# Kernel tuning notes

Measured on AMD Instinct MI355X. Metric: run time of the kernel, lower is better.

The kernel has to match this reference:

```python
import jax, jax.numpy as jnp
import numpy as np

REL_DIM = 1024
NUM_HEADS = 16
HEAD_DIM = REL_DIM // NUM_HEADS
REL_EMB_DIM = 256
B, K = 32, 512
SCALE = 1.0 / float(np.sqrt(HEAD_DIM))


def setup_inputs() -> dict:
    key = jax.random.key(0)
    ks = jax.random.split(key, 7)
    s = 1.0 / float(np.sqrt(REL_DIM))
    return {
        "h_R": jax.random.normal(ks[0], (B, K, REL_DIM), dtype=jnp.float32),
        "R": jax.random.normal(ks[1], (K, REL_EMB_DIM), dtype=jnp.float32),
        "W_q": jax.random.normal(ks[2], (REL_DIM, REL_DIM), dtype=jnp.float32) * s,
        "W_k": jax.random.normal(ks[3], (REL_DIM, REL_DIM), dtype=jnp.float32) * s,
        "W_v": jax.random.normal(ks[4], (REL_DIM, REL_DIM), dtype=jnp.float32) * s,
        "W_o": jax.random.normal(ks[5], (REL_DIM, REL_DIM), dtype=jnp.float32) * s,
        "w_sim": jax.random.normal(ks[6], (NUM_HEADS,), dtype=jnp.float32) * 0.1,
    }


def reference(h_R, R, W_q, W_k, W_v, W_o, w_sim):
    Bb, Kk, _ = h_R.shape
    H, D = NUM_HEADS, HEAD_DIM
    # torch Linear: x @ W.T ; then split heads -> (B, H, K, D)
    def proj(x, W):
        return jnp.einsum('bkd,ed->bke', x, W).reshape(Bb, Kk, H, D).transpose(0, 2, 1, 3)
    q = proj(h_R, W_q)
    k = proj(h_R, W_k)
    v = proj(h_R, W_v)
    attn = jnp.einsum('bhqd,bhkd->bhqk', q, k) * SCALE
    # cosine-similarity bias (batch-independent): (H, K, K)
    R_norm = R / jnp.maximum(jnp.linalg.norm(R, axis=-1, keepdims=True), 1e-12)
    sim = R_norm @ R_norm.T  # (K, K)
    bias = w_sim[:, None, None] * sim[None]  # (H, K, K)
    attn = attn + bias[None]
    alpha = jax.nn.softmax(attn, axis=-1)
    out = jnp.einsum('bhqk,bhkd->bhqd', alpha, v)
    out = out.transpose(0, 2, 1, 3).reshape(Bb, Kk, H * D)
    return jnp.einsum('bkd,ed->bke', out, W_o)
```

## Files before the change

### kernel.cpp

```cpp
#include <hip/hip_runtime.h>

#define SEQK 512
#define NH 16
#define HD 64
#define RD 1024
#define BBATCH 32
#define QK_SCALE 0.125f
#define LOG2E 1.4426950408889634f

typedef unsigned short u16;
using bf16x8 = __attribute__((ext_vector_type(8))) short;
using f32x4  = __attribute__((ext_vector_type(4))) float;

__device__ __forceinline__ u16 f2bf(float f) {
  unsigned u = __float_as_uint(f);
  u += 0x7FFFu + ((u >> 16) & 1u);
  return (u16)(u >> 16);
}
__device__ __forceinline__ float bf2f(u16 v) {
  return __uint_as_float(((unsigned)v) << 16);
}
__device__ __forceinline__ float fexp2(float x) {
  float r;
  asm("v_exp_f32 %0, %1" : "=v"(r) : "v"(x));
  return r;
}

__device__ __forceinline__ void async_cp16(const void* g, void* l) {
  __builtin_amdgcn_global_load_lds(
      (__attribute__((address_space(1))) void*)(void*)g,
      (__attribute__((address_space(3))) void*)l,
      16, 0, 0);
}

__global__ void convert_kernel(const float* __restrict__ hR,
                               const float* __restrict__ Wq, const float* __restrict__ Wk,
                               const float* __restrict__ Wv, const float* __restrict__ Wo,
                               u16* __restrict__ hR16,
                               u16* __restrict__ Wq16, u16* __restrict__ Wk16,
                               u16* __restrict__ Wv16, u16* __restrict__ Wo16) {
  size_t i4 = (size_t)blockIdx.x * blockDim.x + threadIdx.x;
  size_t e = i4 * 4;
  const float* src; u16* dst; size_t off;
  if (e < 16777216u) { src = hR; dst = hR16; off = e; }
  else {
    size_t r = e - 16777216u;
    int w = (int)(r >> 20);
    off = r & 1048575u;
    src = (w == 0 ? Wq : w == 1 ? Wk : w == 2 ? Wv : Wo);
    dst = (w == 0 ? Wq16 : w == 1 ? Wk16 : w == 2 ? Wv16 : Wo16);
  }
  float4 v = *(const float4*)(src + off);
  ushort4 o;
  o.x = f2bf(v.x); o.y = f2bf(v.y); o.z = f2bf(v.z); o.w = f2bf(v.w);
  *(ushort4*)(dst + off) = o;
}

__global__ void rnorm_kernel(const float* __restrict__ R, float* __restrict__ Rn) {
  int row = blockIdx.x;
  int lane = threadIdx.x;
  float4 v = *(const float4*)(R + (size_t)row * 256 + lane * 4);
  float ss = v.x * v.x + v.y * v.y + v.z * v.z + v.w * v.w;
  for (int off = 32; off; off >>= 1) ss += __shfl_xor(ss, off);
  float s = 1.0f / fmaxf(sqrtf(ss), 1e-12f);
  float4 o = {v.x * s, v.y * s, v.z * s, v.w * s};
  *(float4*)(Rn + (size_t)row * 256 + lane * 4) = o;
}

__global__ void sim_kernel(const float* __restrict__ Rn, u16* __restrict__ sim16) {
  __shared__ float Rl[16 * 256];
  int i0 = blockIdx.x * 16;
  int t = threadIdx.x;
  #pragma unroll
  for (int i = 0; i < 4; i++) {
    int f = t + i * 256;
    *(float4*)&Rl[f * 4] = *(const float4*)(Rn + (size_t)i0 * 256 + f * 4);
  }
  __syncthreads();
  for (int jj = 0; jj < 2; jj++) {
    int j = jj * 256 + t;
    float acc[16];
    #pragma unroll
    for (int i = 0; i < 16; i++) acc[i] = 0.f;
    for (int c = 0; c < 64; c++) {
      float4 rv = *(const float4*)(Rn + (size_t)j * 256 + c * 4);
      #pragma unroll
      for (int i = 0; i < 16; i++) {
        float4 a = *(const float4*)&Rl[i * 256 + c * 4];
        acc[i] += a.x * rv.x + a.y * rv.y + a.z * rv.z + a.w * rv.w;
      }
    }
    #pragma unroll
    for (int i = 0; i < 16; i++) sim16[(size_t)(i0 + i) * 512 + j] = f2bf(acc[i]);
  }
}

template <int MODE>
__global__ __launch_bounds__(256)
void gemm_kernel(const u16* __restrict__ A,
                 const u16* __restrict__ B0, const u16* __restrict__ B1,
                 const u16* __restrict__ B2,
                 u16* __restrict__ q16, u16* __restrict__ k16, u16* __restrict__ v16,
                 float* __restrict__ outF) {
  __shared__ u16 Alds[128 * 32];
  __shared__ u16 Blds[128 * 32];
  int tid = threadIdx.x;
  int wave = tid >> 6, lane = tid & 63;
  int wm = wave & 1, wn = wave >> 1;
  int lr = lane & 15, qd = lane >> 4;
  int mb = blockIdx.x * 128;
  int ny = blockIdx.y;

  const u16* Bmat;
  int nbmat;
  if (MODE == 0) {
    int wsel = ny >> 3;
    Bmat = (wsel == 0 ? B0 : wsel == 1 ? B1 : B2);
    nbmat = (ny & 7) * 128;
  } else {
    Bmat = B0;
    nbmat = ny * 128;
  }

  f32x4 zero = {0.f, 0.f, 0.f, 0.f};
  f32x4 acc[4][4];
  #pragma unroll
  for (int i = 0; i < 4; i++)
    #pragma unroll
    for (int j = 0; j < 4; j++) acc[i][j] = zero;

  for (int kb = 0; kb < 1024; kb += 32) {
    #pragma unroll
    for (int j = 0; j < 2; j++) {
      int r = (wave * 2 + j) * 16 + (lane >> 2);
      int c = (lane & 3) ^ ((r >> 1) & 3);
      async_cp16(A + (size_t)(mb + r) * 1024 + kb + c * 8,
                 &Alds[(wave * 2 + j) * 512]);
      async_cp16(Bmat + (size_t)(nbmat + r) * 1024 + kb + c * 8,
                 &Blds[(wave * 2 + j) * 512]);
    }
    __syncthreads();

    bf16x8 af[4], bf[4];
    #pragma unroll
    for (int mi = 0; mi < 4; mi++) {
      int ra = wm * 64 + mi * 16 + lr;
      af[mi] = *(const bf16x8*)&Alds[ra * 32 + ((qd ^ ((ra >> 1) & 3)) << 3)];
      int rb = wn * 64 + mi * 16 + lr;
      bf[mi] = *(const bf16x8*)&Blds[rb * 32 + ((qd ^ ((rb >> 1) & 3)) << 3)];
    }
    #pragma unroll
    for (int mi = 0; mi < 4; mi++)
      #pragma unroll
      for (int ni = 0; ni < 4; ni++)
        acc[mi][ni] = __builtin_amdgcn_mfma_f32_16x16x32_bf16(af[mi], bf[ni],
                                                              acc[mi][ni], 0, 0, 0);
    __syncthreads();
  }

  if (MODE == 0) {
    int wsel = ny >> 3;
    u16* dst = (wsel == 0 ? q16 : wsel == 1 ? k16 : v16);
    float scl = (wsel == 0) ? QK_SCALE * LOG2E : 1.0f;
    #pragma unroll
    for (int mi = 0; mi < 4; mi++) {
      int m = mb + wm * 64 + mi * 16 + qd * 4;
      int b = m >> 9, kk = m & 511;
      #pragma unroll
      for (int ni = 0; ni < 4; ni++) {
        int n = nbmat + wn * 64 + ni * 16 + lr;
        int h = n >> 6, d = n & 63;
        u16* p = dst + ((size_t)(b * 16 + h) * 512 + kk) * 64 + d;
        #pragma unroll
        for (int r = 0; r < 4; r++) p[(size_t)r * 64] = f2bf(acc[mi][ni][r] * scl);
      }
    }
  } else {
    #pragma unroll
    for (int mi = 0; mi < 4; mi++) {
      int m = mb + wm * 64 + mi * 16 + qd * 4;
      #pragma unroll
      for (int ni = 0; ni < 4; ni++) {
        int n = ny * 128 + wn * 64 + ni * 16 + lr;
        #pragma unroll
        for (int r = 0; r < 4; r++) outF[(size_t)(m + r) * 1024 + n] = acc[mi][ni][r];
      }
    }
  }
}

__global__ void vtrans_kernel(const u16* __restrict__ v16, u16* __restrict__ vt16) {
  __shared__ u16 tile[64 * 72];
  int kt = blockIdx.x;
  int bh = blockIdx.y;
  int t = threadIdx.x;
  const u16* src = v16 + ((size_t)bh * 512 + kt * 64) * 64;
  #pragma unroll
  for (int j = 0; j < 2; j++) {
    int linear = j * 2048 + t * 8;
    int kr = linear >> 6, d0 = linear & 63;
    bf16x8 vv = *(const bf16x8*)(src + (size_t)kr * 64 + d0);
    #pragma unroll
    for (int e = 0; e < 8; e++) tile[kr * 72 + d0 + e] = (u16)vv[e];
  }
  __syncthreads();
  #pragma unroll
  for (int j = 0; j < 2; j++) {
    int linear = j * 2048 + t * 8;
    int dr = linear >> 6, k0 = linear & 63;
    bf16x8 ov;
    #pragma unroll
    for (int e = 0; e < 8; e++) ov[e] = (short)tile[(k0 + e) * 72 + dr];
    *(bf16x8*)(vt16 + ((size_t)bh * 64 + dr) * 512 + kt * 64 + k0) = ov;
  }
}

__global__ __launch_bounds__(256, 2)
void attn_kernel(const u16* __restrict__ q16, const u16* __restrict__ k16,
                 const u16* __restrict__ vt16, const u16* __restrict__ sim16,
                 const float* __restrict__ wsim, u16* __restrict__ attn16) {
  __shared__ u16 Kbuf[2][128 * 64];
  __shared__ u16 Vbuf[2][64 * 128];
  __shared__ u16 Plds[4 * 16 * 128];

  int id = blockIdx.x;
  int xcd = id & 7;
  int j = id >> 3;
  int qt = j & 7;
  int bh = xcd * 64 + (j >> 3);
  int b = bh >> 4, h = bh & 15;

  int tid = threadIdx.x;
  int wave = tid >> 6, lane = tid & 63;
  int lr = lane & 15, qd = lane >> 4;
  int qrb = qt * 64 + wave * 16;
  u16* Pw = &Plds[wave * 2048];

  const u16* qp = q16 + ((size_t)bh * 512 + qrb + lr) * 64 + qd * 8;
  bf16x8 aq0 = *(const bf16x8*)qp;
  bf16x8 aq1 = *(const bf16x8*)(qp + 32);

  float ws = wsim[h] * LOG2E;
  int row0 = qrb + qd * 4;

  f32x4 zero = {0.f, 0.f, 0.f, 0.f};
  f32x4 o[4];
  #pragma unroll
  for (int nt = 0; nt < 4; nt++) o[nt] = zero;
  float m_run[4] = {-1e30f, -1e30f, -1e30f, -1e30f};
  float l_run[4] = {0.f, 0.f, 0.f, 0.f};

  const u16* kbase = k16 + (size_t)bh * 512 * 64;
  const u16* vbase = vt16 + (size_t)bh * 64 * 512;

  auto stage = [&](int nb, int ck) {
    int k0 = ck * 128;
    #pragma unroll
    for (int jj = 0; jj < 4; jj++) {
      int rbase = wave * 32 + jj * 8;
      int r = rbase + (lane >> 3);
      int c = (lane & 7) ^ (r & 7);
      async_cp16(kbase + (size_t)(k0 + r) * 64 + c * 8, &Kbuf[nb][rbase * 64]);
    }
    #pragma unroll
    for (int jj = 0; jj < 4; jj++) {
      int dbase = wave * 16 + jj * 4;
      int d = dbase + (lane >> 4);
      int c = (lane & 15) ^ (d & 15);
      async_cp16(vbase + (size_t)d * 512 + k0 + c * 8, &Vbuf[nb][dbase * 128]);
    }
  };

  stage(0, 0);
  __syncthreads();

  int cb = 0;
  for (int ck = 0; ck < 4; ck++) {
    int k0 = ck * 128;

    ushort4 braw[8];
    #pragma unroll
    for (int jt = 0; jt < 8; jt++) {
      int kl = jt * 16 + lr;
      braw[jt] = *(const ushort4*)(sim16 + (size_t)(k0 + kl) * 512 + row0);
    }
    __builtin_amdgcn_sched_barrier(0);
    if (ck < 3) stage(cb ^ 1, ck + 1);

    const u16* Kc = &Kbuf[cb][0];
    const u16* Vc = &Vbuf[cb][0];

    __builtin_amdgcn_s_setprio(1);
    f32x4 s[8];
    #pragma unroll
    for (int jt = 0; jt < 8; jt++) {
      int kl = jt * 16 + lr;
      ushort4 b4 = braw[jt];
      f32x4 t = {ws * bf2f(b4.x), ws * bf2f(b4.y), ws * bf2f(b4.z), ws * bf2f(b4.w)};
      const u16* krow = Kc + kl * 64;
      int sw = kl & 7;
      bf16x8 kf0 = *(const bf16x8*)(krow + ((qd ^ sw) << 3));
      bf16x8 kf1 = *(const bf16x8*)(krow + (((qd + 4) ^ sw) << 3));
      t = __builtin_amdgcn_mfma_f32_16x16x32_bf16(aq0, kf0, t, 0, 0, 0);
      t = __builtin_amdgcn_mfma_f32_16x16x32_bf16(aq1, kf1, t, 0, 0, 0);
      s[jt] = t;
    }
    __builtin_amdgcn_s_setprio(0);

    float mnew[4], alpha[4], csum[4];
    #pragma unroll
    for (int r = 0; r < 4; r++) {
      float m = s[0][r];
      #pragma unroll
      for (int jt = 1; jt < 8; jt++) m = fmaxf(m, s[jt][r]);
      m = fmaxf(m, __shfl_xor(m, 1));
      m = fmaxf(m, __shfl_xor(m, 2));
      m = fmaxf(m, __shfl_xor(m, 4));
      m = fmaxf(m, __shfl_xor(m, 8));
      mnew[r] = fmaxf(m_run[r], m);
      alpha[r] = fexp2(m_run[r] - mnew[r]);
      m_run[r] = mnew[r];
      csum[r] = 0.f;
    }
    #pragma unroll
    for (int jt = 0; jt < 8; jt++)
      #pragma unroll
      for (int r = 0; r < 4; r++) {
        float e = fexp2(s[jt][r] - mnew[r]);
        s[jt][r] = e;
        csum[r] += e;
      }
    #pragma unroll
    for (int r = 0; r < 4; r++) {
      float t = csum[r];
      t += __shfl_xor(t, 1); t += __shfl_xor(t, 2);
      t += __shfl_xor(t, 4); t += __shfl_xor(t, 8);
      l_run[r] = l_run[r] * alpha[r] + t;
    }
    #pragma unroll
    for (int jt = 0; jt < 8; jt++) {
      int c = jt * 2 + (lr >> 3);
      int e = lr & 7;
      #pragma unroll
      for (int r = 0; r < 4; r++) {
        int row = qd * 4 + r;
        Pw[row * 128 + ((c ^ row) & 15) * 8 + e] = f2bf(s[jt][r]);
      }
    }
    #pragma unroll
    for (int nt = 0; nt < 4; nt++)
      #pragma unroll
      for (int r = 0; r < 4; r++) o[nt][r] *= alpha[r];
    __builtin_amdgcn_s_setprio(1);
    #pragma unroll
    for (int ks = 0; ks < 4; ks++) {
      bf16x8 ap = *(const bf16x8*)&Pw[lr * 128 + (((ks * 4 + qd) ^ lr) & 15) * 8];
      #pragma unroll
      for (int nt = 0; nt < 4; nt++) {
        int d = nt * 16 + lr;
        bf16x8 vf = *(const bf16x8*)&Vc[d * 128 + (((ks * 4 + qd) ^ (d & 15)) << 3)];
        o[nt] = __builtin_amdgcn_mfma_f32_16x16x32_bf16(ap, vf, o[nt], 0, 0, 0);
      }
    }
    __builtin_amdgcn_s_setprio(0);
    if (ck < 3) __syncthreads();
    cb ^= 1;
  }

  float inv[4];
  #pragma unroll
  for (int r = 0; r < 4; r++) inv[r] = 1.0f / l_run[r];
  u16* Ow = Pw;
  #pragma unroll
  for (int nt = 0; nt < 4; nt++)
    #pragma unroll
    for (int r = 0; r < 4; r++)
      Ow[(qd * 4 + r) * 72 + nt * 16 + lr] = f2bf(o[nt][r] * inv[r]);
  #pragma unroll
  for (int it = 0; it < 2; it++) {
    int row = it * 8 + (lane >> 3);
    int seg = lane & 7;
    bf16x8 val = *(const bf16x8*)&Ow[row * 72 + seg * 8];
    *(bf16x8*)(attn16 + ((size_t)b * 512 + qrb + row) * 1024 + h * 64 + seg * 8) = val;
  }
}

extern "C" void kernel_launch(void* const* d_in, const int* in_sizes, int n_in,
                              void* d_out, int out_size, void* d_ws, size_t ws_size,
                              hipStream_t stream) {
  const float* hR  = (const float*)d_in[0];
  const float* R   = (const float*)d_in[1];
  const float* Wq  = (const float*)d_in[2];
  const float* Wk  = (const float*)d_in[3];
  const float* Wv  = (const float*)d_in[4];
  const float* Wo  = (const float*)d_in[5];
  const float* wsm = (const float*)d_in[6];
  float* out = (float*)d_out;

  const size_t NE = 16777216;
  u16* ws16   = (u16*)d_ws;
  u16* hR16   = ws16;
  u16* attn16 = ws16;
  u16* q16    = ws16 + NE;
  u16* k16    = ws16 + 2 * NE;
  u16* v16    = ws16 + 3 * NE;
  u16* vt16   = ws16 + 4 * NE;
  u16* Wq16   = ws16 + 5 * NE;
  u16* Wk16   = Wq16 + 1048576;
  u16* Wv16   = Wk16 + 1048576;
  u16* Wo16   = Wv16 + 1048576;
  u16* sim16  = Wo16 + 1048576;
  float* Rn   = (float*)(sim16 + 262144);

  convert_kernel<<<20480, 256, 0, stream>>>(hR, Wq, Wk, Wv, Wo,
                                            hR16, Wq16, Wk16, Wv16, Wo16);
  rnorm_kernel<<<512, 64, 0, stream>>>(R, Rn);
  sim_kernel<<<32, 256, 0, stream>>>(Rn, sim16);
  gemm_kernel<0><<<dim3(128, 24), 256, 0, stream>>>(hR16, Wq16, Wk16, Wv16,
                                                    q16, k16, v16, nullptr);
  vtrans_kernel<<<dim3(8, 512), 256, 0, stream>>>(v16, vt16);
  attn_kernel<<<4096, 256, 0, stream>>>(q16, k16, vt16, sim16, wsm, attn16);
  gemm_kernel<1><<<dim3(128, 8), 256, 0, stream>>>(attn16, Wo16, nullptr, nullptr,
                                                   nullptr, nullptr, nullptr, out);
}
```

Baseline: 498.7 us.

## Rework attention kernel around 32x32 MFMA with register-resident probabilities

The attention kernel switches from 16x16x32 to 32x32x16 bf16 MFMA, computing the transposed score tile so each lane owns one query row. The softmax row max and sum then need only a permlane32 swap instead of shuffle trees. The probabilities are packed to bf16 and fed straight into the PV MFMA from registers via permlane32_swap, removing the LDS write/read round-trip for P. Each block now covers 128 query rows with 64-key chunks and a smaller shared buffer, targeting 3 blocks per CU. The similarity bias is read row-major, which relies on the similarity matrix being symmetric.

```diff
diff --git a/kernel.cpp b/kernel.cpp
--- a/kernel.cpp
+++ b/kernel.cpp
@@ -9,8 +9,10 @@
 #define LOG2E 1.4426950408889634f
 
 typedef unsigned short u16;
+typedef unsigned int u32;
 using bf16x8 = __attribute__((ext_vector_type(8))) short;
 using f32x4  = __attribute__((ext_vector_type(4))) float;
+using f32x16 = __attribute__((ext_vector_type(16))) float;
 
 __device__ __forceinline__ u16 f2bf(float f) {
   unsigned u = __float_as_uint(f);
@@ -24,6 +26,20 @@
   float r;
   asm("v_exp_f32 %0, %1" : "=v"(r) : "v"(x));
   return r;
+}
+__device__ __forceinline__ u32 pkbf(float lo, float hi) {
+  u32 r;
+  asm("v_cvt_pk_bf16_f32 %0, %1, %2" : "=v"(r) : "v"(lo), "v"(hi));
+  return r;
+}
+__device__ __forceinline__ void plswap(u32& a, u32& b) {
+#if __has_builtin(__builtin_amdgcn_permlane32_swap)
+  typedef int v2i __attribute__((ext_vector_type(2)));
+  v2i r = __builtin_amdgcn_permlane32_swap((int)a, (int)b, false, false);
+  a = (u32)r[0]; b = (u32)r[1];
+#else
+  asm volatile("v_permlane32_swap_b32 %0, %1" : "+v"(a), "+v"(b));
+#endif
 }
 
 __device__ __forceinline__ void async_cp16(const void* g, void* l) {
@@ -215,173 +231,176 @@
   }
 }
 
-__global__ __launch_bounds__(256, 2)
+__global__ __launch_bounds__(256, 3)
 void attn_kernel(const u16* __restrict__ q16, const u16* __restrict__ k16,
                  const u16* __restrict__ vt16, const u16* __restrict__ sim16,
                  const float* __restrict__ wsim, u16* __restrict__ attn16) {
-  __shared__ u16 Kbuf[2][128 * 64];
-  __shared__ u16 Vbuf[2][64 * 128];
-  __shared__ u16 Plds[4 * 16 * 128];
+  __shared__ u16 smem[16384];
 
   int id = blockIdx.x;
   int xcd = id & 7;
   int j = id >> 3;
-  int qt = j & 7;
-  int bh = xcd * 64 + (j >> 3);
+  int qt = j & 3;
+  int bh = xcd * 64 + (j >> 2);
   int b = bh >> 4, h = bh & 15;
 
   int tid = threadIdx.x;
   int wave = tid >> 6, lane = tid & 63;
-  int lr = lane & 15, qd = lane >> 4;
-  int qrb = qt * 64 + wave * 16;
-  u16* Pw = &Plds[wave * 2048];
-
-  const u16* qp = q16 + ((size_t)bh * 512 + qrb + lr) * 64 + qd * 8;
-  bf16x8 aq0 = *(const bf16x8*)qp;
-  bf16x8 aq1 = *(const bf16x8*)(qp + 32);
+  int l31 = lane & 31, hi = lane >> 5;
+  int qb = qt * 128 + wave * 32;
+
+  const u16* qp = q16 + ((size_t)bh * 512 + qb + l31) * 64 + hi * 8;
+  bf16x8 aq[4];
+  #pragma unroll
+  for (int ds = 0; ds < 4; ds++) aq[ds] = *(const bf16x8*)(qp + ds * 16);
 
   float ws = wsim[h] * LOG2E;
-  int row0 = qrb + qd * 4;
-
-  f32x4 zero = {0.f, 0.f, 0.f, 0.f};
-  f32x4 o[4];
-  #pragma unroll
-  for (int nt = 0; nt < 4; nt++) o[nt] = zero;
-  float m_run[4] = {-1e30f, -1e30f, -1e30f, -1e30f};
-  float l_run[4] = {0.f, 0.f, 0.f, 0.f};
+
+  f32x16 o[2];
+  #pragma unroll
+  for (int dt = 0; dt < 2; dt++)
+    #pragma unroll
+    for (int r = 0; r < 16; r++) o[dt][r] = 0.f;
+  float m_run = -1e30f, l_run = 0.f;
 
   const u16* kbase = k16 + (size_t)bh * 512 * 64;
   const u16* vbase = vt16 + (size_t)bh * 64 * 512;
 
   auto stage = [&](int nb, int ck) {
-    int k0 = ck * 128;
-    #pragma unroll
-    for (int jj = 0; jj < 4; jj++) {
-      int rbase = wave * 32 + jj * 8;
-      int r = rbase + (lane >> 3);
-      int c = (lane & 7) ^ (r & 7);
-      async_cp16(kbase + (size_t)(k0 + r) * 64 + c * 8, &Kbuf[nb][rbase * 64]);
-    }
-    #pragma unroll
-    for (int jj = 0; jj < 4; jj++) {
-      int dbase = wave * 16 + jj * 4;
-      int d = dbase + (lane >> 4);
-      int c = (lane & 15) ^ (d & 15);
-      async_cp16(vbase + (size_t)d * 512 + k0 + c * 8, &Vbuf[nb][dbase * 128]);
+    int k0 = ck * 64;
+    u16* kd = smem + nb * 4096;
+    u16* vd = smem + 8192 + nb * 4096;
+    #pragma unroll
+    for (int it = 0; it < 2; it++) {
+      int idx = it * 256 + wave * 64 + lane;
+      int r = idx >> 3, c8 = idx & 7;
+      async_cp16(kbase + (size_t)(k0 + r) * 64 + ((c8 ^ (r & 7)) << 3),
+                 kd + (it * 256 + wave * 64) * 8);
+    }
+    #pragma unroll
+    for (int it = 0; it < 2; it++) {
+      int idx = it * 256 + wave * 64 + lane;
+      int dr = idx >> 3, c8 = idx & 7;
+      async_cp16(vbase + (size_t)dr * 512 + k0 + ((c8 ^ (dr & 7)) << 3),
+                 vd + (it * 256 + wave * 64) * 8);
     }
   };
 
   stage(0, 0);
   __syncthreads();
 
-  int cb = 0;
-  for (int ck = 0; ck < 4; ck++) {
-    int k0 = ck * 128;
-
-    ushort4 braw[8];
-    #pragma unroll
-    for (int jt = 0; jt < 8; jt++) {
-      int kl = jt * 16 + lr;
-      braw[jt] = *(const ushort4*)(sim16 + (size_t)(k0 + kl) * 512 + row0);
-    }
+  int cur = 0;
+  for (int ck = 0; ck < 8; ck++) {
+    int k0 = ck * 64;
+
+    uint2 braw[8];
+    #pragma unroll
+    for (int kb = 0; kb < 2; kb++)
+      #pragma unroll
+      for (int g = 0; g < 4; g++)
+        braw[kb * 4 + g] = *(const uint2*)(sim16 + (size_t)(qb + l31) * 512 +
+                                           k0 + kb * 32 + g * 8 + hi * 4);
     __builtin_amdgcn_sched_barrier(0);
-    if (ck < 3) stage(cb ^ 1, ck + 1);
-
-    const u16* Kc = &Kbuf[cb][0];
-    const u16* Vc = &Vbuf[cb][0];
-
+    if (ck < 7) stage(cur ^ 1, ck + 1);
+
+    const u16* Kc = smem + cur * 4096;
+    const u16* Vc = smem + 8192 + cur * 4096;
+
+    f32x16 s[2];
     __builtin_amdgcn_s_setprio(1);
-    f32x4 s[8];
-    #pragma unroll
-    for (int jt = 0; jt < 8; jt++) {
-      int kl = jt * 16 + lr;
-      ushort4 b4 = braw[jt];
-      f32x4 t = {ws * bf2f(b4.x), ws * bf2f(b4.y), ws * bf2f(b4.z), ws * bf2f(b4.w)};
-      const u16* krow = Kc + kl * 64;
-      int sw = kl & 7;
-      bf16x8 kf0 = *(const bf16x8*)(krow + ((qd ^ sw) << 3));
-      bf16x8 kf1 = *(const bf16x8*)(krow + (((qd + 4) ^ sw) << 3));
-      t = __builtin_amdgcn_mfma_f32_16x16x32_bf16(aq0, kf0, t, 0, 0, 0);
-      t = __builtin_amdgcn_mfma_f32_16x16x32_bf16(aq1, kf1, t, 0, 0, 0);
-      s[jt] = t;
+    #pragma unroll
+    for (int kb = 0; kb < 2; kb++) {
+      f32x16 acc;
+      #pragma unroll
+      for (int r = 0; r < 16; r++) {
+        u32 w = ((r >> 1) & 1) ? braw[kb * 4 + (r >> 2)].y
+                               : braw[kb * 4 + (r >> 2)].x;
+        acc[r] = ws * __uint_as_float((r & 1) ? (w & 0xFFFF0000u) : (w << 16));
+      }
+      int koff = kb * 32 + l31;
+      #pragma unroll
+      for (int ds = 0; ds < 4; ds++) {
+        bf16x8 kf = *(const bf16x8*)&Kc[koff * 64 + (((ds * 2 + hi) ^ (koff & 7)) << 3)];
+        acc = __builtin_amdgcn_mfma_f32_32x32x16_bf16(kf, aq[ds], acc, 0, 0, 0);
+      }
+      s[kb] = acc;
     }
     __builtin_amdgcn_s_setprio(0);
 
-    float mnew[4], alpha[4], csum[4];
-    #pragma unroll
-    for (int r = 0; r < 4; r++) {
-      float m = s[0][r];
-      #pragma unroll
-      for (int jt = 1; jt < 8; jt++) m = fmaxf(m, s[jt][r]);
-      m = fmaxf(m, __shfl_xor(m, 1));
-      m = fmaxf(m, __shfl_xor(m, 2));
-      m = fmaxf(m, __shfl_xor(m, 4));
-      m = fmaxf(m, __shfl_xor(m, 8));
-      mnew[r] = fmaxf(m_run[r], m);
-      alpha[r] = fexp2(m_run[r] - mnew[r]);
-      m_run[r] = mnew[r];
-      csum[r] = 0.f;
-    }
-    #pragma unroll
-    for (int jt = 0; jt < 8; jt++)
-      #pragma unroll
-      for (int r = 0; r < 4; r++) {
-        float e = fexp2(s[jt][r] - mnew[r]);
-        s[jt][r] = e;
-        csum[r] += e;
-      }
-    #pragma unroll
-    for (int r = 0; r < 4; r++) {
-      float t = csum[r];
-      t += __shfl_xor(t, 1); t += __shfl_xor(t, 2);
-      t += __shfl_xor(t, 4); t += __shfl_xor(t, 8);
-      l_run[r] = l_run[r] * alpha[r] + t;
-    }
-    #pragma unroll
-    for (int jt = 0; jt < 8; jt++) {
-      int c = jt * 2 + (lr >> 3);
-      int e = lr & 7;
-      #pragma unroll
-      for (int r = 0; r < 4; r++) {
-        int row = qd * 4 + r;
-        Pw[row * 128 + ((c ^ row) & 15) * 8 + e] = f2bf(s[jt][r]);
-      }
-    }
-    #pragma unroll
-    for (int nt = 0; nt < 4; nt++)
-      #pragma unroll
-      for (int r = 0; r < 4; r++) o[nt][r] *= alpha[r];
+    float v8[8];
+    #pragma unroll
+    for (int i = 0; i < 8; i++)
+      v8[i] = fmaxf(fmaxf(s[0][i], s[0][i + 8]), fmaxf(s[1][i], s[1][i + 8]));
+    float m_in = fmaxf(fmaxf(fmaxf(v8[0], v8[1]), fmaxf(v8[2], v8[3])),
+                       fmaxf(fmaxf(v8[4], v8[5]), fmaxf(v8[6], v8[7])));
+    u32 xa = __float_as_uint(m_in), xb = __float_as_uint(m_in);
+    plswap(xa, xb);
+    float m_tile = fmaxf(__uint_as_float(xa), __uint_as_float(xb));
+    float mnew = fmaxf(m_run, m_tile);
+    float alpha = fexp2(m_run - mnew);
+    m_run = mnew;
+
+    float c0 = 0.f, c1 = 0.f, c2 = 0.f, c3 = 0.f;
+    #pragma unroll
+    for (int kb = 0; kb < 2; kb++)
+      #pragma unroll
+      for (int i = 0; i < 16; i++) {
+        float e = fexp2(s[kb][i] - mnew);
+        s[kb][i] = e;
+        if ((i & 3) == 0) c0 += e; else if ((i & 3) == 1) c1 += e;
+        else if ((i & 3) == 2) c2 += e; else c3 += e;
+      }
+    float cs = (c0 + c1) + (c2 + c3);
+    u32 ya = __float_as_uint(cs), yb = __float_as_uint(cs);
+    plswap(ya, yb);
+    float cs_tot = __uint_as_float(ya) + __uint_as_float(yb);
+    l_run = l_run * alpha + cs_tot;
+
+    #pragma unroll
+    for (int dt = 0; dt < 2; dt++) o[dt] *= alpha;
+
     __builtin_amdgcn_s_setprio(1);
     #pragma unroll
     for (int ks = 0; ks < 4; ks++) {
-      bf16x8 ap = *(const bf16x8*)&Pw[lr * 128 + (((ks * 4 + qd) ^ lr) & 15) * 8];
-      #pragma unroll
-      for (int nt = 0; nt < 4; nt++) {
-        int d = nt * 16 + lr;
-        bf16x8 vf = *(const bf16x8*)&Vc[d * 128 + (((ks * 4 + qd) ^ (d & 15)) << 3)];
-        o[nt] = __builtin_amdgcn_mfma_f32_16x16x32_bf16(ap, vf, o[nt], 0, 0, 0);
+      int kb = ks >> 1, j4 = (ks & 1) * 8;
+      u32 a0 = pkbf(s[kb][j4 + 0], s[kb][j4 + 1]);
+      u32 a1 = pkbf(s[kb][j4 + 2], s[kb][j4 + 3]);
+      u32 b0 = pkbf(s[kb][j4 + 4], s[kb][j4 + 5]);
+      u32 b1 = pkbf(s[kb][j4 + 6], s[kb][j4 + 7]);
+      plswap(a0, b0);
+      plswap(a1, b1);
+      union { u32 w[4]; bf16x8 v; } U;
+      U.w[0] = a0; U.w[1] = a1; U.w[2] = b0; U.w[3] = b1;
+      #pragma unroll
+      for (int dt = 0; dt < 2; dt++) {
+        int dr = dt * 32 + l31;
+        bf16x8 vf = *(const bf16x8*)&Vc[dr * 64 + (((ks * 2 + hi) ^ (dr & 7)) << 3)];
+        o[dt] = __builtin_amdgcn_mfma_f32_32x32x16_bf16(vf, U.v, o[dt], 0, 0, 0);
       }
     }
     __builtin_amdgcn_s_setprio(0);
-    if (ck < 3) __syncthreads();
-    cb ^= 1;
-  }
-
-  float inv[4];
-  #pragma unroll
-  for (int r = 0; r < 4; r++) inv[r] = 1.0f / l_run[r];
-  u16* Ow = Pw;
-  #pragma unroll
-  for (int nt = 0; nt < 4; nt++)
-    #pragma unroll
-    for (int r = 0; r < 4; r++)
-      Ow[(qd * 4 + r) * 72 + nt * 16 + lr] = f2bf(o[nt][r] * inv[r]);
-  #pragma unroll
-  for (int it = 0; it < 2; it++) {
-    int row = it * 8 + (lane >> 3);
-    int seg = lane & 7;
+
+    __syncthreads();
+    cur ^= 1;
+  }
+
+  float linv = 1.0f / l_run;
+  u16* Ow = smem + wave * 2304;
+  #pragma unroll
+  for (int dt = 0; dt < 2; dt++)
+    #pragma unroll
+    for (int g = 0; g < 4; g++) {
+      u32 w0 = pkbf(o[dt][4 * g + 0] * linv, o[dt][4 * g + 1] * linv);
+      u32 w1 = pkbf(o[dt][4 * g + 2] * linv, o[dt][4 * g + 3] * linv);
+      uint2 pr; pr.x = w0; pr.y = w1;
+      *(uint2*)&Ow[l31 * 72 + dt * 32 + g * 8 + hi * 4] = pr;
+    }
+  #pragma unroll
+  for (int i = 0; i < 4; i++) {
+    int idx = i * 64 + lane;
+    int row = idx >> 3, seg = idx & 7;
     bf16x8 val = *(const bf16x8*)&Ow[row * 72 + seg * 8];
-    *(bf16x8*)(attn16 + ((size_t)b * 512 + qrb + row) * 1024 + h * 64 + seg * 8) = val;
+    *(bf16x8*)(attn16 + ((size_t)b * 512 + qb + row) * 1024 + h * 64 + seg * 8) = val;
   }
 }
 
@@ -419,7 +438,7 @@
   gemm_kernel<0><<<dim3(128, 24), 256, 0, stream>>>(hR16, Wq16, Wk16, Wv16,
                                                     q16, k16, v16, nullptr);
   vtrans_kernel<<<dim3(8, 512), 256, 0, stream>>>(v16, vt16);
-  attn_kernel<<<4096, 256, 0, stream>>>(q16, k16, vt16, sim16, wsm, attn16);
+  attn_kernel<<<2048, 256, 0, stream>>>(q16, k16, vt16, sim16, wsm, attn16);
   gemm_kernel<1><<<dim3(128, 8), 256, 0, stream>>>(attn16, Wo16, nullptr, nullptr,
                                                    nullptr, nullptr, nullptr, out);
 }
```

After: 454.4 us. 8.9% less time.
